# Optimization experiments

Measured on AMD Instinct MI355X. Metric: run time of the kernel, lower is better.

The kernel has to match this reference:

```python
import jax, jax.numpy as jnp
import numpy as np


def setup_inputs() -> dict:
    key = jax.random.key(0)
    ks = jax.random.split(key, 6)
    C, C8, W, H, B = 512, 64, 64, 64, 4
    x = jax.random.normal(ks[0], (B, C, W, H), dtype=jnp.float32)
    Wf = jax.random.normal(ks[1], (C8, C), dtype=jnp.float32) * (1.0 / np.sqrt(C))
    Wg = jax.random.normal(ks[2], (C8, C), dtype=jnp.float32) * (1.0 / np.sqrt(C))
    Wh = jax.random.normal(ks[3], (C8, C), dtype=jnp.float32) * (1.0 / np.sqrt(C))
    Wv = jax.random.normal(ks[4], (C, C8), dtype=jnp.float32) * (1.0 / np.sqrt(C8))
    gamma = jax.random.normal(ks[5], (1,), dtype=jnp.float32)
    return {"x": x, "Wf": Wf, "Wg": Wg, "Wh": Wh, "Wv": Wv, "gamma": gamma}


def reference(x, Wf, Wg, Wh, Wv, gamma):
    b, c, w, h = x.shape
    n = w * h
    xf = x.reshape(b, c, n)                       # [b, c, n]
    # 1x1 convs == channel-mixing GEMMs
    f = jnp.einsum('oc,bcn->bon', Wf, xf)         # [b, c8, n]
    g = jnp.einsum('oc,bcn->bon', Wg, xf)         # [b, c8, n]
    hmap = jnp.einsum('oc,bcn->bon', Wh, xf)      # [b, c8, n]
    # attn_map[b, i, j] = sum_c f[b, c, i] * g[b, c, j]  (f permuted as in torch)
    attn = jnp.einsum('bci,bcj->bij', f, g)       # [b, n, n]
    # unconventional softmax over dim=1 (rows / the i axis)
    attn = jax.nn.softmax(attn, axis=1)
    sa = jnp.einsum('bcn,bnj->bcj', hmap, attn)   # [b, c8, n]
    sa = sa.reshape(b, -1, w, h)                  # [b, c8, w, h]
    sa = jnp.einsum('oc,bcwh->bowh', Wv, sa)      # [b, c, w, h]
    out = sa * gamma[0] + x
    return out, sa
```

## Files before the change

### kernel.cpp

```cpp
#include <hip/hip_runtime.h>
#include <cstddef>

#define BB 4
#define CC 512
#define NN 4096

using half8  = __attribute__((ext_vector_type(8))) _Float16;
using fp16x2 = __attribute__((ext_vector_type(2))) __fp16;
using short8 = __attribute__((ext_vector_type(8))) short;
using us8    = __attribute__((ext_vector_type(8))) unsigned short;
using f32x4  = __attribute__((ext_vector_type(4))) float;
using f32x16 = __attribute__((ext_vector_type(16))) float;

__device__ __forceinline__ unsigned short f2bf(float x) {
    unsigned int u = __float_as_uint(x);
    u += 0x7fffu + ((u >> 16) & 1u);
    return (unsigned short)(u >> 16);
}

__global__ __launch_bounds__(256) void prep_kernel(
    const float* __restrict__ Wf, const float* __restrict__ Wg,
    const float* __restrict__ Wh, const float* __restrict__ Wv,
    _Float16* __restrict__ Wc16, _Float16* __restrict__ Wv16)
{
    int idx = blockIdx.x * 256 + threadIdx.x;
    int stride = gridDim.x * 256;
    const int N1 = 192 * 512, N2 = 512 * 64;
    for (int i = idx; i < N1 + N2; i += stride) {
        if (i < N1) {
            int row = i >> 9, c = i & 511;
            const float* src = (row < 64) ? Wf : ((row < 128) ? Wg : Wh);
            float sc = (row >= 64 && row < 128) ? 1.4426950408889634f : 1.0f;
            Wc16[i] = (_Float16)(sc * src[(row & 63) * 512 + c]);
        } else {
            int k = i - N1;
            Wv16[k] = (_Float16)Wv[k];
        }
    }
}

__global__ __launch_bounds__(256) void proj_kernel(
    const float* __restrict__ x, const _Float16* __restrict__ Wc16,
    _Float16* __restrict__ Kf, _Float16* __restrict__ Qf,
    unsigned short* __restrict__ Vt)
{
    __shared__ float xsT[2][32][68];
    const int t    = threadIdx.x;
    const int w    = t >> 6;
    const int lane = t & 63;
    const int lh   = lane & 15;
    const int qd   = lane >> 4;
    const int b    = blockIdx.x >> 7;
    const int i0   = (blockIdx.x & 127) << 5;

    f32x4 acc[3][2];
    #pragma unroll
    for (int ot = 0; ot < 3; ot++)
        #pragma unroll
        for (int it = 0; it < 2; it++) { acc[ot][it][0]=0.f; acc[ot][it][1]=0.f; acc[ot][it][2]=0.f; acc[ot][it][3]=0.f; }

    const int ti8 = t & 7;
    const int tc2 = t >> 3;
    const float* xbase = x + (size_t)b*CC*NN + i0 + ti8*4;
    const _Float16* wbase = Wc16 + (size_t)(w*48 + lh)*512 + qd*8;

    float4 st0, st1;
    half8  wcur[2][3], wnxt[2][3];

#define LOADX(ck) do {                                                        \
    st0 = *(const float4*)(xbase + (size_t)((ck)*64 + tc2)*NN);               \
    st1 = *(const float4*)(xbase + (size_t)((ck)*64 + 32 + tc2)*NN);          \
} while (0)
#define STOREX(p_) do {                                                       \
    xsT[p_][ti8*4+0][tc2]    = st0.x; xsT[p_][ti8*4+1][tc2]    = st0.y;       \
    xsT[p_][ti8*4+2][tc2]    = st0.z; xsT[p_][ti8*4+3][tc2]    = st0.w;       \
    xsT[p_][ti8*4+0][32+tc2] = st1.x; xsT[p_][ti8*4+1][32+tc2] = st1.y;       \
    xsT[p_][ti8*4+2][32+tc2] = st1.z; xsT[p_][ti8*4+3][32+tc2] = st1.w;       \
} while (0)
#define LOADW(ck, WD) do {                                                    \
    _Pragma("unroll")                                                         \
    for (int ks_ = 0; ks_ < 2; ks_++)                                         \
        _Pragma("unroll")                                                     \
        for (int ot_ = 0; ot_ < 3; ot_++)                                     \
            WD[ks_][ot_] = *(const half8*)(wbase + (size_t)(ot_*16)*512 + (ck)*64 + ks_*32); \
} while (0)

    LOADX(0); STOREX(0);
    LOADW(0, wcur);
    __syncthreads();

    #pragma unroll
    for (int ck = 0; ck < 8; ck++) {
        const int p = ck & 1;
        if (ck < 7) { LOADX(ck + 1); LOADW(ck + 1, wnxt); }

        #pragma unroll
        for (int ks = 0; ks < 2; ks++) {
            half8 xf[2];
            #pragma unroll
            for (int it = 0; it < 2; it++) {
                const float* xr = &xsT[p][it*16 + lh][ks*32 + qd*8];
                f32x4 xa = *(const f32x4*)xr;
                f32x4 xb = *(const f32x4*)(xr + 4);
                union { fp16x2 h2[4]; half8 h8; } u;
                u.h2[0] = __builtin_amdgcn_cvt_pkrtz(xa[0], xa[1]);
                u.h2[1] = __builtin_amdgcn_cvt_pkrtz(xa[2], xa[3]);
                u.h2[2] = __builtin_amdgcn_cvt_pkrtz(xb[0], xb[1]);
                u.h2[3] = __builtin_amdgcn_cvt_pkrtz(xb[2], xb[3]);
                xf[it] = u.h8;
            }
            #pragma unroll
            for (int ot = 0; ot < 3; ot++)
                #pragma unroll
                for (int it = 0; it < 2; it++)
                    acc[ot][it] = __builtin_amdgcn_mfma_f32_16x16x32_f16(wcur[ks][ot], xf[it], acc[ot][it], 0, 0, 0);
        }

        if (ck < 7) {
            STOREX(p ^ 1);
            #pragma unroll
            for (int ks_ = 0; ks_ < 2; ks_++)
                #pragma unroll
                for (int ot_ = 0; ot_ < 3; ot_++)
                    wcur[ks_][ot_] = wnxt[ks_][ot_];
        }
        __syncthreads();
    }
#undef LOADX
#undef STOREX
#undef LOADW

    #pragma unroll
    for (int ot = 0; ot < 3; ot++) {
        int g16 = w*3 + ot;
        int m   = g16 >> 2;
        int obase = (g16 & 3)*16 + qd*4;
        #pragma unroll
        for (int it = 0; it < 2; it++) {
            int ig = i0 + it*16 + lh;
            #pragma unroll
            for (int r = 0; r < 4; r++) {
                float v = acc[ot][it][r];
                int ol = obase + r;
                if (m == 0)       Kf[((size_t)b*NN + ig)*64 + ol] = (_Float16)v;
                else if (m == 1)  Qf[((size_t)b*NN + ig)*64 + ol] = (_Float16)v;
                else              Vt[((size_t)b*64 + ol)*NN + ig] = f2bf(v);
            }
        }
    }
}

template<int SPLITS>
__global__ __launch_bounds__(256, 4) void attn_kernel(
    const _Float16* __restrict__ Kf, const _Float16* __restrict__ Qf,
    const unsigned short* __restrict__ Vt,
    _Float16* __restrict__ Po16, float* __restrict__ Pl)
{
    static_assert(NN % SPLITS == 0, "split");
    constexpr int KS  = NN / SPLITS;
    constexpr int NCH = KS / 64;

    __shared__ __align__(16) unsigned short Kb2[2][64*64];
    __shared__ __align__(16) unsigned short Vb2[2][64*64];

    const int t    = threadIdx.x;
    const int wv   = t >> 6;
    const int lane = t & 63;
    const int il   = lane & 31;
    const int h    = lane >> 5;

    const int p  = blockIdx.x;
    const int v  = (p & 7) * (SPLITS * 16) + (p >> 3);
    const int jt = v & 31;
    const int bs = v >> 5;
    const int b  = bs / SPLITS;
    const int s  = bs % SPLITS;
    const int j0w  = jt*128 + wv*32;
    const int koff = s * KS;

    half8 qfr[4];
    {
        const _Float16* qp = Qf + ((size_t)b*NN + j0w + il)*64 + h*8;
        #pragma unroll
        for (int sl = 0; sl < 4; sl++) qfr[sl] = *(const half8*)(qp + sl*16);
    }

    f32x16 o_acc[2];
    #pragma unroll
    for (int dt = 0; dt < 2; dt++)
        #pragma unroll
        for (int r = 0; r < 16; r++) o_acc[dt][r] = 0.f;
    float l4[4] = {0.f, 0.f, 0.f, 0.f};

    const int slot0 = t, slot1 = 256 + t;
    const int ik0 = slot0 >> 3, sw0 = ((slot0 & 7) ^ (ik0 & 7)) << 3;
    const int ik1 = slot1 >> 3, sw1 = ((slot1 & 7) ^ (ik1 & 7)) << 3;
    const _Float16*       gk0 = Kf + ((size_t)b*NN + koff + ik0)*64 + sw0;
    const _Float16*       gk1 = Kf + ((size_t)b*NN + koff + ik1)*64 + sw1;
    const unsigned short* gv0 = Vt + ((size_t)b*64 + ik0)*NN + koff + sw0;
    const unsigned short* gv1 = Vt + ((size_t)b*64 + ik1)*NN + koff + sw1;

#define STAGE(ck, pb) do {                                                          \
    const size_t o64_ = (size_t)(ck)*64;                                            \
    __builtin_amdgcn_global_load_lds(                                               \
        (const __attribute__((address_space(1))) void*)(gk0 + o64_*64),             \
        (__attribute__((address_space(3))) void*)&Kb2[pb][(wv*64)*8], 16, 0, 0);    \
    __builtin_amdgcn_global_load_lds(                                               \
        (const __attribute__((address_space(1))) void*)(gk1 + o64_*64),             \
        (__attribute__((address_space(3))) void*)&Kb2[pb][(256 + wv*64)*8], 16, 0, 0); \
    __builtin_amdgcn_global_load_lds(                                               \
        (const __attribute__((address_space(1))) void*)(gv0 + o64_),                \
        (__attribute__((address_space(3))) void*)&Vb2[pb][(wv*64)*8], 16, 0, 0);    \
    __builtin_amdgcn_global_load_lds(                                               \
        (const __attribute__((address_space(1))) void*)(gv1 + o64_),                \
        (__attribute__((address_space(3))) void*)&Vb2[pb][(256 + wv*64)*8], 16, 0, 0); \
    } while (0)

    STAGE(0, 0);
    __syncthreads();

    for (int ck = 0; ck < NCH; ck++) {
        const int cb = ck & 1;
        if (ck + 1 < NCH) STAGE(ck + 1, cb ^ 1);

        const unsigned short* Kb = Kb2[cb];
        const unsigned short* Vb = Vb2[cb];

        #pragma unroll
        for (int isub = 0; isub < 2; isub++) {
            const int irow = isub*32 + il;
            const unsigned short* kr = Kb + irow*64;
            f32x16 sc;
            #pragma unroll
            for (int r = 0; r < 16; r++) sc[r] = 0.f;
            __builtin_amdgcn_s_setprio(1);
            #pragma unroll
            for (int sl = 0; sl < 4; sl++) {
                half8 kf = *(const half8*)(kr + (((sl*2 + h) ^ (irow & 7)) << 3));
                sc = __builtin_amdgcn_mfma_f32_32x32x16_f16(kf, qfr[sl], sc, 0, 0, 0);
            }
            __builtin_amdgcn_s_setprio(0);

            #pragma unroll
            for (int r = 0; r < 16; r++) sc[r] = exp2f(sc[r]);
            #pragma unroll
            for (int r = 0; r < 16; r++) l4[r & 3] += sc[r];

            unsigned wA[8];
            #pragma unroll
            for (int k = 0; k < 8; k++)
                asm("v_cvt_pk_bf16_f32 %0, %1, %2" : "=v"(wA[k]) : "v"(sc[2*k]), "v"(sc[2*k+1]));
            asm("v_permlane32_swap_b32 %0, %1" : "+v"(wA[0]), "+v"(wA[2]));
            asm("v_permlane32_swap_b32 %0, %1" : "+v"(wA[1]), "+v"(wA[3]));
            asm("v_permlane32_swap_b32 %0, %1" : "+v"(wA[4]), "+v"(wA[6]));
            asm("v_permlane32_swap_b32 %0, %1" : "+v"(wA[5]), "+v"(wA[7]));

            union { unsigned u[4]; short8 s8; } pa0, pa1;
            pa0.u[0]=wA[0]; pa0.u[1]=wA[1]; pa0.u[2]=wA[2]; pa0.u[3]=wA[3];
            pa1.u[0]=wA[4]; pa1.u[1]=wA[5]; pa1.u[2]=wA[6]; pa1.u[3]=wA[7];

            __builtin_amdgcn_s_setprio(1);
            #pragma unroll
            for (int isl = 0; isl < 2; isl++) {
                const short8 paf = isl ? pa1.s8 : pa0.s8;
                const int vc = isub*4 + isl*2 + h;
                #pragma unroll
                for (int dt = 0; dt < 2; dt++) {
                    const int drow = dt*32 + il;
                    short8 vf = *(const short8*)(Vb + drow*64 + ((vc ^ (drow & 7)) << 3));
                    o_acc[dt] = __builtin_amdgcn_mfma_f32_32x32x16_bf16(paf, vf, o_acc[dt], 0, 0, 0);
                }
            }
            __builtin_amdgcn_s_setprio(0);
        }
        __syncthreads();
    }
#undef STAGE

    float l_acc  = (l4[0] + l4[1]) + (l4[2] + l4[3]);
    float l_full = l_acc + __shfl_xor(l_acc, 32);
    float inv = 1.0f / l_full;

    const size_t pbase = (size_t)(s*4 + b)*NN + j0w;
    #pragma unroll
    for (int r = 0; r < 16; r++) {
        const int jr = (r & 3) + 8*(r >> 2) + 4*h;
        const float invr = __shfl(inv, jr);
        #pragma unroll
        for (int dt = 0; dt < 2; dt++)
            Po16[(pbase + jr)*64 + dt*32 + il] = (_Float16)(o_acc[dt][r] * invr);
    }
    if (h == 0) Pl[pbase + il] = l_full;
}

template<int SPLITS>
__global__ __launch_bounds__(256) void outproj_kernel(
    const _Float16* __restrict__ Po16, const float* __restrict__ Pl,
    const _Float16* __restrict__ Wv16,
    const float* __restrict__ x, const float* __restrict__ gamma,
    float* __restrict__ out1, float* __restrict__ out2)
{
    __shared__ float Osh[4][16][36];
    const int t    = threadIdx.x;
    const int w    = t >> 6;
    const int lane = t & 63;
    const int lh   = lane & 15;
    const int qd   = lane >> 4;
    const int b    = blockIdx.x >> 7;
    const int j0   = (blockIdx.x & 127) << 5;
    const float g  = gamma[0];

    half8 sb[2][2];
    #pragma unroll
    for (int jt2 = 0; jt2 < 2; jt2++) {
        const int j = j0 + jt2*16 + lh;
        float os[16];
        #pragma unroll
        for (int k = 0; k < 16; k++) os[k] = 0.f;
        float lsum = 0.f;
        #pragma unroll
        for (int s = 0; s < SPLITS; s++) {
            size_t base = ((size_t)(s*4 + b)*NN + j);
            half8 v0 = *(const half8*)(Po16 + base*64 + qd*8);
            half8 v1 = *(const half8*)(Po16 + base*64 + qd*8 + 32);
            float l = Pl[base];
            #pragma unroll
            for (int k = 0; k < 8; k++) {
                os[k]   = fmaf(l, (float)v0[k], os[k]);
                os[8+k] = fmaf(l, (float)v1[k], os[8+k]);
            }
            lsum += l;
        }
        float inv = 1.0f / lsum;
        union { fp16x2 h2[4]; half8 h8; } u0, u1;
        #pragma unroll
        for (int k = 0; k < 4; k++) {
            u0.h2[k] = __builtin_amdgcn_cvt_pkrtz(os[2*k]*inv,   os[2*k+1]*inv);
            u1.h2[k] = __builtin_amdgcn_cvt_pkrtz(os[8+2*k]*inv, os[8+2*k+1]*inv);
        }
        sb[jt2][0] = u0.h8;
        sb[jt2][1] = u1.h8;
    }

    const int o_loc8 = lane >> 3;
    const int j4     = (lane & 7) * 4;

    #pragma unroll 2
    for (int ot8 = 0; ot8 < 8; ot8++) {
        const int ot = w*8 + ot8;
        const size_t wbase = (size_t)(ot*16 + lh)*64 + qd*8;
        half8 a0 = *(const half8*)(Wv16 + wbase);
        half8 a1 = *(const half8*)(Wv16 + wbase + 32);

        f32x4 acc[2];
        #pragma unroll
        for (int jt2 = 0; jt2 < 2; jt2++) {
            acc[jt2][0]=0.f; acc[jt2][1]=0.f; acc[jt2][2]=0.f; acc[jt2][3]=0.f;
            acc[jt2] = __builtin_amdgcn_mfma_f32_16x16x32_f16(a0, sb[jt2][0], acc[jt2], 0, 0, 0);
            acc[jt2] = __builtin_amdgcn_mfma_f32_16x16x32_f16(a1, sb[jt2][1], acc[jt2], 0, 0, 0);
        }

        #pragma unroll
        for (int jt2 = 0; jt2 < 2; jt2++)
            #pragma unroll
            for (int r = 0; r < 4; r++)
                Osh[w][qd*4 + r][jt2*16 + lh] = acc[jt2][r];
        asm volatile("s_waitcnt lgkmcnt(0)" ::: "memory");

        #pragma unroll
        for (int rr2 = 0; rr2 < 2; rr2++) {
            const int o_loc = o_loc8 + 8*rr2;
            f32x4 v = *(const f32x4*)&Osh[w][o_loc][j4];
            const int o  = ot*16 + o_loc;
            const size_t idx = ((size_t)b*CC + o)*NN + j0 + j4;
            f32x4 xv = *(const f32x4*)(x + idx);
            *(f32x4*)(out2 + idx) = v;
            f32x4 r1;
            r1[0] = fmaf(g, v[0], xv[0]); r1[1] = fmaf(g, v[1], xv[1]);
            r1[2] = fmaf(g, v[2], xv[2]); r1[3] = fmaf(g, v[3], xv[3]);
            *(f32x4*)(out1 + idx) = r1;
        }
        asm volatile("s_waitcnt lgkmcnt(0)" ::: "memory");
    }
}

extern "C" void kernel_launch(void* const* d_in, const int* in_sizes, int n_in,
                              void* d_out, int out_size, void* d_ws, size_t ws_size,
                              hipStream_t stream) {
    const float* x     = (const float*)d_in[0];
    const float* Wf    = (const float*)d_in[1];
    const float* Wg    = (const float*)d_in[2];
    const float* Wh    = (const float*)d_in[3];
    const float* Wv    = (const float*)d_in[4];
    const float* gamma = (const float*)d_in[5];

    float* out1 = (float*)d_out;
    float* out2 = out1 + (size_t)BB*CC*NN;

    const size_t BND = (size_t)BB*NN*64;
    const size_t need8 = BND*2*3 + BND*2*8 + (size_t)8*BB*NN*4
                       + (size_t)192*512*2 + (size_t)512*64*2;
    const int SPL = (ws_size >= need8) ? 8 : 4;

    char* wp = (char*)d_ws;
    _Float16*       Kf   = (_Float16*)wp;        wp += BND*2;
    _Float16*       Qf   = (_Float16*)wp;        wp += BND*2;
    unsigned short* Vt   = (unsigned short*)wp;  wp += BND*2;
    _Float16*       Po16 = (_Float16*)wp;        wp += BND*2*SPL;
    float*          Pl   = (float*)wp;           wp += (size_t)SPL*BB*NN*4;
    _Float16*       Wc16 = (_Float16*)wp;        wp += (size_t)192*512*2;
    _Float16*       Wv16 = (_Float16*)wp;

    prep_kernel<<<dim3(64), dim3(256), 0, stream>>>(Wf, Wg, Wh, Wv, Wc16, Wv16);
    proj_kernel<<<dim3(BB*128), dim3(256), 0, stream>>>(x, Wc16, Kf, Qf, Vt);
    if (SPL == 8) {
        attn_kernel<8><<<dim3(128*8), dim3(256), 0, stream>>>(Kf, Qf, Vt, Po16, Pl);
        outproj_kernel<8><<<dim3(512), dim3(256), 0, stream>>>(Po16, Pl, Wv16, x, gamma, out1, out2);
    } else {
        attn_kernel<4><<<dim3(128*4), dim3(256), 0, stream>>>(Kf, Qf, Vt, Po16, Pl);
        outproj_kernel<4><<<dim3(512), dim3(256), 0, stream>>>(Po16, Pl, Wv16, x, gamma, out1, out2);
    }
}
```

Before: 165.3 us.

## Shrink projection tiles, swizzle block order, drop setprio, relax attention occupancy

The projection kernel now handles 16 spatial positions per block instead of 32 and launches twice as many blocks. Block indices are remapped with an interleaving swizzle, and launch bounds request 4 blocks per SM. This trades per-block weight reuse for more parallelism and occupancy. Separately, the attention kernel drops its s_setprio hints, keeps exp results in a separate array instead of overwriting the score accumulator, and lowers its minimum blocks-per-SM hint from 4 to 3, which frees registers at some cost in latency hiding.

```diff
diff --git a/kernel.cpp b/kernel.cpp
--- a/kernel.cpp
+++ b/kernel.cpp
@@ -39,43 +39,41 @@
     }
 }
 
-__global__ __launch_bounds__(256) void proj_kernel(
+__global__ __launch_bounds__(256, 4) void proj_kernel(
     const float* __restrict__ x, const _Float16* __restrict__ Wc16,
     _Float16* __restrict__ Kf, _Float16* __restrict__ Qf,
     unsigned short* __restrict__ Vt)
 {
-    __shared__ float xsT[2][32][68];
+    __shared__ float xsT[2][16][68];
     const int t    = threadIdx.x;
     const int w    = t >> 6;
     const int lane = t & 63;
     const int lh   = lane & 15;
     const int qd   = lane >> 4;
-    const int b    = blockIdx.x >> 7;
-    const int i0   = (blockIdx.x & 127) << 5;
-
-    f32x4 acc[3][2];
-    #pragma unroll
-    for (int ot = 0; ot < 3; ot++)
-        #pragma unroll
-        for (int it = 0; it < 2; it++) { acc[ot][it][0]=0.f; acc[ot][it][1]=0.f; acc[ot][it][2]=0.f; acc[ot][it][3]=0.f; }
-
-    const int ti8 = t & 7;
-    const int tc2 = t >> 3;
-    const float* xbase = x + (size_t)b*CC*NN + i0 + ti8*4;
+
+    const int g  = blockIdx.x;
+    const int v  = (g & 7) * 128 + (g >> 3);
+    const int b  = v >> 8;
+    const int i0 = (v & 255) << 4;
+
+    f32x4 acc[3];
+    #pragma unroll
+    for (int ot = 0; ot < 3; ot++) { acc[ot][0]=0.f; acc[ot][1]=0.f; acc[ot][2]=0.f; acc[ot][3]=0.f; }
+
+    const int i4 = t & 3;
+    const int cr = t >> 2;
+    const float* xbase = x + (size_t)b*CC*NN + i0 + i4*4;
     const _Float16* wbase = Wc16 + (size_t)(w*48 + lh)*512 + qd*8;
 
-    float4 st0, st1;
+    float4 st0;
     half8  wcur[2][3], wnxt[2][3];
 
 #define LOADX(ck) do {                                                        \
-    st0 = *(const float4*)(xbase + (size_t)((ck)*64 + tc2)*NN);               \
-    st1 = *(const float4*)(xbase + (size_t)((ck)*64 + 32 + tc2)*NN);          \
+    st0 = *(const float4*)(xbase + (size_t)((ck)*64 + cr)*NN);                \
 } while (0)
 #define STOREX(p_) do {                                                       \
-    xsT[p_][ti8*4+0][tc2]    = st0.x; xsT[p_][ti8*4+1][tc2]    = st0.y;       \
-    xsT[p_][ti8*4+2][tc2]    = st0.z; xsT[p_][ti8*4+3][tc2]    = st0.w;       \
-    xsT[p_][ti8*4+0][32+tc2] = st1.x; xsT[p_][ti8*4+1][32+tc2] = st1.y;       \
-    xsT[p_][ti8*4+2][32+tc2] = st1.z; xsT[p_][ti8*4+3][32+tc2] = st1.w;       \
+    xsT[p_][i4*4+0][cr] = st0.x; xsT[p_][i4*4+1][cr] = st0.y;                 \
+    xsT[p_][i4*4+2][cr] = st0.z; xsT[p_][i4*4+3][cr] = st0.w;                 \
 } while (0)
 #define LOADW(ck, WD) do {                                                    \
     _Pragma("unroll")                                                         \
@@ -96,24 +94,18 @@
 
         #pragma unroll
         for (int ks = 0; ks < 2; ks++) {
-            half8 xf[2];
-            #pragma unroll
-            for (int it = 0; it < 2; it++) {
-                const float* xr = &xsT[p][it*16 + lh][ks*32 + qd*8];
-                f32x4 xa = *(const f32x4*)xr;
-                f32x4 xb = *(const f32x4*)(xr + 4);
-                union { fp16x2 h2[4]; half8 h8; } u;
-                u.h2[0] = __builtin_amdgcn_cvt_pkrtz(xa[0], xa[1]);
-                u.h2[1] = __builtin_amdgcn_cvt_pkrtz(xa[2], xa[3]);
-                u.h2[2] = __builtin_amdgcn_cvt_pkrtz(xb[0], xb[1]);
-                u.h2[3] = __builtin_amdgcn_cvt_pkrtz(xb[2], xb[3]);
-                xf[it] = u.h8;
-            }
+            const float* xr = &xsT[p][lh][ks*32 + qd*8];
+            f32x4 xa = *(const f32x4*)xr;
+            f32x4 xb = *(const f32x4*)(xr + 4);
+            union { fp16x2 h2[4]; half8 h8; } u;
+            u.h2[0] = __builtin_amdgcn_cvt_pkrtz(xa[0], xa[1]);
+            u.h2[1] = __builtin_amdgcn_cvt_pkrtz(xa[2], xa[3]);
+            u.h2[2] = __builtin_amdgcn_cvt_pkrtz(xb[0], xb[1]);
+            u.h2[3] = __builtin_amdgcn_cvt_pkrtz(xb[2], xb[3]);
+            half8 xf = u.h8;
             #pragma unroll
             for (int ot = 0; ot < 3; ot++)
-                #pragma unroll
-                for (int it = 0; it < 2; it++)
-                    acc[ot][it] = __builtin_amdgcn_mfma_f32_16x16x32_f16(wcur[ks][ot], xf[it], acc[ot][it], 0, 0, 0);
+                acc[ot] = __builtin_amdgcn_mfma_f32_16x16x32_f16(wcur[ks][ot], xf, acc[ot], 0, 0, 0);
         }
 
         if (ck < 7) {
@@ -135,23 +127,20 @@
         int g16 = w*3 + ot;
         int m   = g16 >> 2;
         int obase = (g16 & 3)*16 + qd*4;
-        #pragma unroll
-        for (int it = 0; it < 2; it++) {
-            int ig = i0 + it*16 + lh;
-            #pragma unroll
-            for (int r = 0; r < 4; r++) {
-                float v = acc[ot][it][r];
-                int ol = obase + r;
-                if (m == 0)       Kf[((size_t)b*NN + ig)*64 + ol] = (_Float16)v;
-                else if (m == 1)  Qf[((size_t)b*NN + ig)*64 + ol] = (_Float16)v;
-                else              Vt[((size_t)b*64 + ol)*NN + ig] = f2bf(v);
-            }
+        int ig = i0 + lh;
+        #pragma unroll
+        for (int r = 0; r < 4; r++) {
+            float vv = acc[ot][r];
+            int ol = obase + r;
+            if (m == 0)       Kf[((size_t)b*NN + ig)*64 + ol] = (_Float16)vv;
+            else if (m == 1)  Qf[((size_t)b*NN + ig)*64 + ol] = (_Float16)vv;
+            else              Vt[((size_t)b*64 + ol)*NN + ig] = f2bf(vv);
         }
     }
 }
 
 template<int SPLITS>
-__global__ __launch_bounds__(256, 4) void attn_kernel(
+__global__ __launch_bounds__(256, 3) void attn_kernel(
     const _Float16* __restrict__ Kf, const _Float16* __restrict__ Qf,
     const unsigned short* __restrict__ Vt,
     _Float16* __restrict__ Po16, float* __restrict__ Pl)
@@ -233,23 +222,22 @@
             f32x16 sc;
             #pragma unroll
             for (int r = 0; r < 16; r++) sc[r] = 0.f;
-            __builtin_amdgcn_s_setprio(1);
             #pragma unroll
             for (int sl = 0; sl < 4; sl++) {
                 half8 kf = *(const half8*)(kr + (((sl*2 + h) ^ (irow & 7)) << 3));
                 sc = __builtin_amdgcn_mfma_f32_32x32x16_f16(kf, qfr[sl], sc, 0, 0, 0);
             }
-            __builtin_amdgcn_s_setprio(0);
-
-            #pragma unroll
-            for (int r = 0; r < 16; r++) sc[r] = exp2f(sc[r]);
-            #pragma unroll
-            for (int r = 0; r < 16; r++) l4[r & 3] += sc[r];
+
+            float pq[16];
+            #pragma unroll
+            for (int r = 0; r < 16; r++) pq[r] = exp2f(sc[r]);
+            #pragma unroll
+            for (int r = 0; r < 16; r++) l4[r & 3] += pq[r];
 
             unsigned wA[8];
             #pragma unroll
             for (int k = 0; k < 8; k++)
-                asm("v_cvt_pk_bf16_f32 %0, %1, %2" : "=v"(wA[k]) : "v"(sc[2*k]), "v"(sc[2*k+1]));
+                asm("v_cvt_pk_bf16_f32 %0, %1, %2" : "=v"(wA[k]) : "v"(pq[2*k]), "v"(pq[2*k+1]));
             asm("v_permlane32_swap_b32 %0, %1" : "+v"(wA[0]), "+v"(wA[2]));
             asm("v_permlane32_swap_b32 %0, %1" : "+v"(wA[1]), "+v"(wA[3]));
             asm("v_permlane32_swap_b32 %0, %1" : "+v"(wA[4]), "+v"(wA[6]));
@@ -259,7 +247,6 @@
             pa0.u[0]=wA[0]; pa0.u[1]=wA[1]; pa0.u[2]=wA[2]; pa0.u[3]=wA[3];
             pa1.u[0]=wA[4]; pa1.u[1]=wA[5]; pa1.u[2]=wA[6]; pa1.u[3]=wA[7];
 
-            __builtin_amdgcn_s_setprio(1);
             #pragma unroll
             for (int isl = 0; isl < 2; isl++) {
                 const short8 paf = isl ? pa1.s8 : pa0.s8;
@@ -271,7 +258,6 @@
                     o_acc[dt] = __builtin_amdgcn_mfma_f32_32x32x16_bf16(paf, vf, o_acc[dt], 0, 0, 0);
                 }
             }
-            __builtin_amdgcn_s_setprio(0);
         }
         __syncthreads();
     }
@@ -370,14 +356,14 @@
         #pragma unroll
         for (int rr2 = 0; rr2 < 2; rr2++) {
             const int o_loc = o_loc8 + 8*rr2;
-            f32x4 v = *(const f32x4*)&Osh[w][o_loc][j4];
+            f32x4 vv = *(const f32x4*)&Osh[w][o_loc][j4];
             const int o  = ot*16 + o_loc;
             const size_t idx = ((size_t)b*CC + o)*NN + j0 + j4;
             f32x4 xv = *(const f32x4*)(x + idx);
-            *(f32x4*)(out2 + idx) = v;
+            *(f32x4*)(out2 + idx) = vv;
             f32x4 r1;
-            r1[0] = fmaf(g, v[0], xv[0]); r1[1] = fmaf(g, v[1], xv[1]);
-            r1[2] = fmaf(g, v[2], xv[2]); r1[3] = fmaf(g, v[3], xv[3]);
+            r1[0] = fmaf(g, vv[0], xv[0]); r1[1] = fmaf(g, vv[1], xv[1]);
+            r1[2] = fmaf(g, vv[2], xv[2]); r1[3] = fmaf(g, vv[3], xv[3]);
             *(f32x4*)(out1 + idx) = r1;
         }
         asm volatile("s_waitcnt lgkmcnt(0)" ::: "memory");
@@ -412,7 +398,7 @@
     _Float16*       Wv16 = (_Float16*)wp;
 
     prep_kernel<<<dim3(64), dim3(256), 0, stream>>>(Wf, Wg, Wh, Wv, Wc16, Wv16);
-    proj_kernel<<<dim3(BB*128), dim3(256), 0, stream>>>(x, Wc16, Kf, Qf, Vt);
+    proj_kernel<<<dim3(BB*256), dim3(256), 0, stream>>>(x, Wc16, Kf, Qf, Vt);
     if (SPL == 8) {
         attn_kernel<8><<<dim3(128*8), dim3(256), 0, stream>>>(Kf, Qf, Vt, Po16, Pl);
         outproj_kernel<8><<<dim3(512), dim3(256), 0, stream>>>(Po16, Pl, Wv16, x, gamma, out1, out2);
```

Result: slower. 174.0 us (+5.2%).
